# Optimization experiments

Hardware: AMD Instinct MI355X
Metric: run time of the kernel (lower is better)

## Reference

```python
import jax, jax.numpy as jnp
import numpy as np

H = 16        # attn_num
A = 64        # head dim
W = 512       # sliding-window length (ar_attn_window_len)
THETA = 10000.0
EPS = 1e-6    # norm_eps


def _rope(x):
    # x: [b, h, s, a]
    s, a = x.shape[2], x.shape[3]
    inv_freq = (1.0 / THETA) ** (jnp.arange(0, a, 2, dtype=jnp.float32) / a)
    freqs = jnp.arange(s, dtype=jnp.float32)[:, None] * inv_freq[None, :]  # [s, a/2]
    cos, sin = jnp.cos(freqs), jnp.sin(freqs)
    x1, x2 = jnp.split(x, 2, axis=-1)
    return jnp.concatenate([x1 * cos + x2 * sin, -x1 * sin + x2 * cos], axis=-1)


def _l2_normalize(x):
    # F.normalize(x, dim=-1, eps): x / max(||x||_2, eps)
    n = jnp.sqrt(jnp.sum(x * x, axis=-1, keepdims=True))
    return x / jnp.maximum(n, EPS)


def setup_inputs() -> dict:
    key = jax.random.key(0)
    kq, kk, kv = jax.random.split(key, 3)
    b, s, d = 2, 4096, H * A
    return {
        "xq": jax.random.normal(kq, (b, s, d), dtype=jnp.float32),
        "xk": jax.random.normal(kk, (b, s, d), dtype=jnp.float32),
        "xv": jax.random.normal(kv, (b, s, d), dtype=jnp.float32),
    }


def reference(xq, xk, xv):
    b, s, d = xq.shape
    to_heads = lambda x: x.reshape(b, s, H, A).transpose(0, 2, 1, 3)  # b h s a
    q, k, v = to_heads(xq), to_heads(xk), to_heads(xv)

    # qk-norm then RoPE, exactly as Attention.forward
    q = _rope(_l2_normalize(q))
    k = _rope(_l2_normalize(k))

    # Block-banded causal sliding-window attention (honors the block sparsity):
    # query block i attends only to key blocks i-1 and i (window = block size W).
    nb = s // W
    qb = q.reshape(b, H, nb, W, A)

    def band(x):
        xb = x.reshape(b, H, nb, W, A)
        xp = jnp.pad(xb, ((0, 0), (0, 0), (1, 0), (0, 0), (0, 0)))  # zero block in front
        return jnp.concatenate([xp[:, :, :-1], xp[:, :, 1:]], axis=3)  # [b,H,nb,2W,A]

    kb, vb = band(k), band(v)

    scale = 1.0 / np.sqrt(A)
    scores = jnp.einsum("bhnqa,bhnka->bhnqk", qb, kb) * scale  # [b,H,nb,W,2W]

    # mask: causal (q >= kv), window (q - kv < W), and kv index in range (>= 0)
    r = jnp.arange(W)
    c = jnp.arange(2 * W)
    diff = r[:, None] - (c[None, :] - W)               # q_global - kv_global
    within = (diff >= 0) & (diff < W)                   # [W, 2W]
    kv_global = (jnp.arange(nb)[:, None] - 1) * W + c[None, :]  # [nb, 2W]
    mask = within[None, :, :] & (kv_global[:, None, :] >= 0)    # [nb, W, 2W]

    scores = jnp.where(mask[None, None], scores, -1e30)
    p = jax.nn.softmax(scores, axis=-1)
    out = jnp.einsum("bhnqk,bhnka->bhnqa", p, vb)       # [b,H,nb,W,A]
    out = out.reshape(b, H, s, A).transpose(0, 2, 1, 3).reshape(b, s, d)
    return out
```

## Files before the change

### kernel.cpp

```cpp
#include <hip/hip_runtime.h>

#define NB 2
#define NH 16
#define SEQ 4096
#define HD 64
#define DIM 1024
#define WIN 512

typedef float f32x16 __attribute__((ext_vector_type(16)));
typedef short bf16x8 __attribute__((ext_vector_type(8)));
typedef unsigned int u32x4 __attribute__((ext_vector_type(4)));
typedef unsigned int u32x2 __attribute__((ext_vector_type(2)));
typedef unsigned short u16;
typedef unsigned int u32;

__device__ __forceinline__ u16 f2bf(float x) {
    u32 u = __float_as_uint(x);
    u += 0x7FFFu + ((u >> 16) & 1u);
    return (u16)(u >> 16);
}

__device__ __forceinline__ u32 cvtpk(float lo, float hi) {
    u32 r;
    asm("v_cvt_pk_bf16_f32 %0, %1, %2" : "=v"(r) : "v"(lo), "v"(hi));
    return r;
}

__device__ __forceinline__ float pexp2(float x) {
    return 1.f + x * (0.69314718f + x * 0.24022651f);
}

__global__ void trig_kernel(float* __restrict__ ct, float* __restrict__ st) {
    int idx = blockIdx.x * 256 + threadIdx.x;
    int s = idx >> 5, j = idx & 31;
    float inv = powf(1.0f / 10000.0f, (float)j * (1.0f / 32.0f));
    float ang = (float)s * inv;
    ct[idx] = cosf(ang);
    st[idx] = sinf(ang);
}

__device__ __forceinline__ void norm_rope_row(const float* __restrict__ row,
                                              const float* __restrict__ cr,
                                              const float* __restrict__ sr,
                                              float scale, u16* __restrict__ dst, int a) {
    float4 u0 = *(const float4*)(row + 8 * a);
    float4 u1 = *(const float4*)(row + 8 * a + 4);
    float4 v0 = *(const float4*)(row + 32 + 8 * a);
    float4 v1 = *(const float4*)(row + 32 + 8 * a + 4);
    float x1[8] = {u0.x, u0.y, u0.z, u0.w, u1.x, u1.y, u1.z, u1.w};
    float x2[8] = {v0.x, v0.y, v0.z, v0.w, v1.x, v1.y, v1.z, v1.w};
    float ss = 0.f;
#pragma unroll
    for (int i = 0; i < 8; ++i) ss += x1[i] * x1[i] + x2[i] * x2[i];
    ss += __shfl_xor(ss, 1);
    ss += __shfl_xor(ss, 2);
    float rn = scale / fmaxf(sqrtf(ss), 1e-6f);
    u16 o1[8], o2[8];
#pragma unroll
    for (int i = 0; i < 8; ++i) {
        float c = cr[8 * a + i], sn = sr[8 * a + i];
        o1[i] = f2bf((x1[i] * c + x2[i] * sn) * rn);
        o2[i] = f2bf((x2[i] * c - x1[i] * sn) * rn);
    }
    uint4 w1, w2;
    w1.x = (u32)o1[0] | ((u32)o1[1] << 16); w1.y = (u32)o1[2] | ((u32)o1[3] << 16);
    w1.z = (u32)o1[4] | ((u32)o1[5] << 16); w1.w = (u32)o1[6] | ((u32)o1[7] << 16);
    w2.x = (u32)o2[0] | ((u32)o2[1] << 16); w2.y = (u32)o2[2] | ((u32)o2[3] << 16);
    w2.z = (u32)o2[4] | ((u32)o2[5] << 16); w2.w = (u32)o2[6] | ((u32)o2[7] << 16);
    *(uint4*)(dst + 8 * a) = w1;
    *(uint4*)(dst + 32 + 8 * a) = w2;
}

__global__ void kv_prep(const float* __restrict__ xk, const float* __restrict__ xv,
                        const float* __restrict__ ctab, const float* __restrict__ stab,
                        u16* __restrict__ Kn, u16* __restrict__ Vt) {
    __shared__ u16 tile[64][66];
    int bid = blockIdx.x;
    int t = threadIdx.x;
    if (bid < 2048) {
        int bh = bid >> 6, stile = bid & 63;
        int b = bh >> 4, h = bh & 15;
        int lr = t >> 2, a = t & 3;
        int s = stile * 64 + lr;
        size_t inoff = ((size_t)(b * SEQ + s)) * DIM + h * HD;
        size_t outoff = ((size_t)bh * SEQ + s) * HD;
        norm_rope_row(xk + inoff, ctab + (size_t)s * 32, stab + (size_t)s * 32, 1.0f,
                      Kn + outoff, a);
    } else {
        int vb = bid - 2048;
        int bh = vb >> 6, stile = vb & 63;
        int b = bh >> 4, h = bh & 15;
        int lr = t >> 2, a = t & 3;
        int s = stile * 64 + lr;
        const float* vrow = xv + ((size_t)(b * SEQ + s)) * DIM + h * HD + 16 * a;
#pragma unroll
        for (int c = 0; c < 4; ++c) {
            float4 w = *(const float4*)(vrow + 4 * c);
            tile[lr][16 * a + 4 * c + 0] = f2bf(w.x);
            tile[lr][16 * a + 4 * c + 1] = f2bf(w.y);
            tile[lr][16 * a + 4 * c + 2] = f2bf(w.z);
            tile[lr][16 * a + 4 * c + 3] = f2bf(w.w);
        }
        __syncthreads();
        int d = t >> 2;
        u32 pk[8];
#pragma unroll
        for (int i = 0; i < 8; ++i) {
            u16 lo = tile[16 * a + 2 * i][d];
            u16 hi = tile[16 * a + 2 * i + 1][d];
            pk[i] = (u32)lo | ((u32)hi << 16);
        }
        u16* dst = Vt + ((size_t)bh * HD + d) * SEQ + stile * 64 + 16 * a;
        *(uint4*)(dst) = make_uint4(pk[0], pk[1], pk[2], pk[3]);
        *(uint4*)(dst + 8) = make_uint4(pk[4], pk[5], pk[6], pk[7]);
    }
}

#define KROW 72
#define VROW 40
__global__ __launch_bounds__(256, 4) void attn_kernel(const float* __restrict__ xq,
                                                      const u16* __restrict__ Kn,
                                                      const u16* __restrict__ Vt,
                                                      const float* __restrict__ ctab,
                                                      const float* __restrict__ stab,
                                                      float* __restrict__ out) {
    __shared__ __align__(16) u16 Kl[2][32 * KROW];
    __shared__ __align__(16) u16 Vl[2][64 * VROW];
    int phys = blockIdx.x;
    int logical = (phys & 7) * 128 + (phys >> 3);
    int bh = logical >> 5, qt = logical & 31;
    int b = bh >> 4, h = bh & 15;
    int tid = threadIdx.x;
    int w = tid >> 6, l = tid & 63;
    int q = l & 31, hi = l >> 5;
    int qblk = qt * 128;
    int qw0 = qblk + w * 32;
    const u16* Kh = Kn + (size_t)bh * SEQ * HD;
    const u16* Vh = Vt + (size_t)bh * HD * SEQ;
    int dq = qw0 + q;

    int bt0 = (qblk - (WIN - 1)) >> 5; if (bt0 < 0) bt0 = 0;
    int bt1 = (qblk + 96) >> 5;

    int krow = tid >> 3, kc = (tid & 7) * 8;
    int vrw  = tid >> 2, vc = (tid & 3) * 8;
    const u16* kgl = Kh + (size_t)krow * HD + kc;
    const u16* vgl = Vh + (size_t)vrw * SEQ + vc;
    u16* kls0 = &Kl[0][krow * KROW + kc];
    u16* kls1 = &Kl[1][krow * KROW + kc];
    u16* vls0 = &Vl[0][vrw * VROW + vc];
    u16* vls1 = &Vl[1][vrw * VROW + vc];

    {
        uint4 gk = *(const uint4*)(kgl + ((size_t)bt0 << 5) * HD);
        uint4 gv = *(const uint4*)(vgl + (bt0 << 5));
        *(uint4*)kls0 = gk;
        *(uint4*)vls0 = gv;
    }

    const float* qrow = xq + ((size_t)(b * SEQ + dq)) * DIM + h * HD;
    float4 xa0 = *(const float4*)(qrow + hi * 8);
    float4 xa1 = *(const float4*)(qrow + hi * 8 + 4);
    float4 xb0 = *(const float4*)(qrow + 16 + hi * 8);
    float4 xb1 = *(const float4*)(qrow + 16 + hi * 8 + 4);
    float4 ya0 = *(const float4*)(qrow + 32 + hi * 8);
    float4 ya1 = *(const float4*)(qrow + 36 + hi * 8);
    float4 yb0 = *(const float4*)(qrow + 48 + hi * 8);
    float4 yb1 = *(const float4*)(qrow + 52 + hi * 8);
    auto d4 = [](float4 v) { return v.x * v.x + v.y * v.y + v.z * v.z + v.w * v.w; };
    float ss = d4(xa0) + d4(xa1) + d4(xb0) + d4(xb1) + d4(ya0) + d4(ya1) + d4(yb0) + d4(yb1);
    ss += __shfl_xor(ss, 32);
    float rn = (0.125f * 1.44269504f) / fmaxf(sqrtf(ss), 1e-6f);
    const float* crp = ctab + (size_t)dq * 32;
    const float* srp = stab + (size_t)dq * 32;
    float4 ca0 = *(const float4*)(crp + hi * 8);
    float4 ca1 = *(const float4*)(crp + hi * 8 + 4);
    float4 cb0 = *(const float4*)(crp + 16 + hi * 8);
    float4 cb1 = *(const float4*)(crp + 16 + hi * 8 + 4);
    float4 sa0 = *(const float4*)(srp + hi * 8);
    float4 sa1 = *(const float4*)(srp + hi * 8 + 4);
    float4 sb0 = *(const float4*)(srp + 16 + hi * 8);
    float4 sb1 = *(const float4*)(srp + 16 + hi * 8 + 4);
    auto mk1 = [&](float4 x0, float4 x1f, float4 y0, float4 y1f,
                   float4 c0, float4 c1, float4 s0, float4 s1) -> bf16x8 {
        u32x4 r;
        r[0] = cvtpk((x0.x * c0.x + y0.x * s0.x) * rn, (x0.y * c0.y + y0.y * s0.y) * rn);
        r[1] = cvtpk((x0.z * c0.z + y0.z * s0.z) * rn, (x0.w * c0.w + y0.w * s0.w) * rn);
        r[2] = cvtpk((x1f.x * c1.x + y1f.x * s1.x) * rn, (x1f.y * c1.y + y1f.y * s1.y) * rn);
        r[3] = cvtpk((x1f.z * c1.z + y1f.z * s1.z) * rn, (x1f.w * c1.w + y1f.w * s1.w) * rn);
        return __builtin_bit_cast(bf16x8, r);
    };
    auto mk2 = [&](float4 x0, float4 x1f, float4 y0, float4 y1f,
                   float4 c0, float4 c1, float4 s0, float4 s1) -> bf16x8 {
        u32x4 r;
        r[0] = cvtpk((y0.x * c0.x - x0.x * s0.x) * rn, (y0.y * c0.y - x0.y * s0.y) * rn);
        r[1] = cvtpk((y0.z * c0.z - x0.z * s0.z) * rn, (y0.w * c0.w - x0.w * s0.w) * rn);
        r[2] = cvtpk((y1f.x * c1.x - x1f.x * s1.x) * rn, (y1f.y * c1.y - x1f.y * s1.y) * rn);
        r[3] = cvtpk((y1f.z * c1.z - x1f.z * s1.z) * rn, (y1f.w * c1.w - x1f.w * s1.w) * rn);
        return __builtin_bit_cast(bf16x8, r);
    };
    bf16x8 qf0 = mk1(xa0, xa1, ya0, ya1, ca0, ca1, sa0, sa1);
    bf16x8 qf1 = mk1(xb0, xb1, yb0, yb1, cb0, cb1, sb0, sb1);
    bf16x8 qf2 = mk2(xa0, xa1, ya0, ya1, ca0, ca1, sa0, sa1);
    bf16x8 qf3 = mk2(xb0, xb1, yb0, yb1, cb0, cb1, sb0, sb1);

    f32x16 acc0, acc1;
#pragma unroll
    for (int i = 0; i < 16; ++i) { acc0[i] = 0.f; acc1[i] = 0.f; }
    float l_ = 0.f;

    int tw0 = (qw0 - (WIN - 1)) >> 5; if (tw0 < 0) tw0 = 0;
    int tw1 = qw0 >> 5;

    const u16* krd0 = &Kl[0][q * KROW + hi * 8];
    const u16* krd1 = &Kl[1][q * KROW + hi * 8];
    const u16* vrd0a = &Vl[0][q * VROW + hi * 8];
    const u16* vrd0b = &Vl[0][(32 + q) * VROW + hi * 8];
    const u16* vrd1a = &Vl[1][q * VROW + hi * 8];
    const u16* vrd1b = &Vl[1][(32 + q) * VROW + hi * 8];

    __syncthreads();

    int c = 0;
    for (int t = bt0; t <= bt1; ++t) {
        int kv0 = t << 5;
        bool more = t < bt1;
        uint4 gk, gv;
        if (more) {
            gk = *(const uint4*)(kgl + ((size_t)(kv0 + 32)) * HD);
            gv = *(const uint4*)(vgl + (kv0 + 32));
        }
        __builtin_amdgcn_sched_barrier(0);

        if (t >= tw0 && t <= tw1) {
            bool mask = (t == tw0) || (t == tw1);
            const u16* kr = c ? krd1 : krd0;
            const u16* va = c ? vrd1a : vrd0a;
            const u16* vb = c ? vrd1b : vrd0b;

            bf16x8 k0 = *(const bf16x8*)(kr);
            bf16x8 k1 = *(const bf16x8*)(kr + 16);
            bf16x8 k2 = *(const bf16x8*)(kr + 32);
            bf16x8 k3 = *(const bf16x8*)(kr + 48);

            f32x16 st;
#pragma unroll
            for (int i = 0; i < 16; ++i) st[i] = 0.f;
            __builtin_amdgcn_s_setprio(1);
            st = __builtin_amdgcn_mfma_f32_32x32x16_bf16(k0, qf0, st, 0, 0, 0);
            st = __builtin_amdgcn_mfma_f32_32x32x16_bf16(k1, qf1, st, 0, 0, 0);
            st = __builtin_amdgcn_mfma_f32_32x32x16_bf16(k2, qf2, st, 0, 0, 0);
            st = __builtin_amdgcn_mfma_f32_32x32x16_bf16(k3, qf3, st, 0, 0, 0);
            __builtin_amdgcn_s_setprio(0);

            bf16x8 va0 = *(const bf16x8*)(va);
            bf16x8 va1 = *(const bf16x8*)(va + 16);
            bf16x8 vb0 = *(const bf16x8*)(vb);
            bf16x8 vb1 = *(const bf16x8*)(vb + 16);

            int base = dq - (kv0 + 4 * hi);
            u32 wd[8];
            float l0 = 0.f, l1 = 0.f;
#pragma unroll
            for (int i = 0; i < 8; ++i) {
                int r0 = 2 * i, r1 = 2 * i + 1;
                float e0 = pexp2(st[r0]);
                float e1 = pexp2(st[r1]);
                if (mask) {
                    int k0off = (r0 & 3) + 8 * (r0 >> 2);
                    int k1off = (r1 & 3) + 8 * (r1 >> 2);
                    e0 = ((u32)(base - k0off) < (u32)WIN) ? e0 : 0.f;
                    e1 = ((u32)(base - k1off) < (u32)WIN) ? e1 : 0.f;
                }
                l0 += e0; l1 += e1;
                wd[i] = cvtpk(e0, e1);
            }
            l_ += l0 + l1;

            u32x4 b1, b2;
#if __has_builtin(__builtin_amdgcn_permlane32_swap)
            u32x2 sA = __builtin_amdgcn_permlane32_swap(wd[0], wd[2], false, false);
            u32x2 sB = __builtin_amdgcn_permlane32_swap(wd[1], wd[3], false, false);
            u32x2 sC = __builtin_amdgcn_permlane32_swap(wd[4], wd[6], false, false);
            u32x2 sD = __builtin_amdgcn_permlane32_swap(wd[5], wd[7], false, false);
            b1 = (u32x4){ sA[0], sB[0], sA[1], sB[1] };
            b2 = (u32x4){ sC[0], sD[0], sC[1], sD[1] };
#else
            u32 e0 = __shfl_xor(hi ? wd[0] : wd[2], 32);
            u32 e1 = __shfl_xor(hi ? wd[1] : wd[3], 32);
            u32 e2 = __shfl_xor(hi ? wd[4] : wd[6], 32);
            u32 e3 = __shfl_xor(hi ? wd[5] : wd[7], 32);
            b1 = (u32x4){ hi ? e0 : wd[0], hi ? e1 : wd[1], hi ? wd[2] : e0, hi ? wd[3] : e1 };
            b2 = (u32x4){ hi ? e2 : wd[4], hi ? e3 : wd[5], hi ? wd[6] : e2, hi ? wd[7] : e3 };
#endif
            bf16x8 pb1 = __builtin_bit_cast(bf16x8, b1);
            bf16x8 pb2 = __builtin_bit_cast(bf16x8, b2);

            __builtin_amdgcn_s_setprio(1);
            acc0 = __builtin_amdgcn_mfma_f32_32x32x16_bf16(va0, pb1, acc0, 0, 0, 0);
            acc0 = __builtin_amdgcn_mfma_f32_32x32x16_bf16(va1, pb2, acc0, 0, 0, 0);
            acc1 = __builtin_amdgcn_mfma_f32_32x32x16_bf16(vb0, pb1, acc1, 0, 0, 0);
            acc1 = __builtin_amdgcn_mfma_f32_32x32x16_bf16(vb1, pb2, acc1, 0, 0, 0);
            __builtin_amdgcn_s_setprio(0);
        }

        if (more) {
            *(uint4*)(c ? kls0 : kls1) = gk;
            *(uint4*)(c ? vls0 : vls1) = gv;
            __syncthreads();
        }
        c ^= 1;
    }

    l_ += __shfl_xor(l_, 32);
    float inv = 1.0f / l_;
    float* orow = out + ((size_t)(b * SEQ + dq)) * DIM + h * HD;
#pragma unroll
    for (int g = 0; g < 4; ++g) {
        float4 v0 = { acc0[4 * g + 0] * inv, acc0[4 * g + 1] * inv,
                      acc0[4 * g + 2] * inv, acc0[4 * g + 3] * inv };
        float4 v1 = { acc1[4 * g + 0] * inv, acc1[4 * g + 1] * inv,
                      acc1[4 * g + 2] * inv, acc1[4 * g + 3] * inv };
        *(float4*)(orow + 8 * g + 4 * hi) = v0;
        *(float4*)(orow + 32 + 8 * g + 4 * hi) = v1;
    }
}

extern "C" void kernel_launch(void* const* d_in, const int* in_sizes, int n_in,
                              void* d_out, int out_size, void* d_ws, size_t ws_size,
                              hipStream_t stream) {
    (void)in_sizes; (void)n_in; (void)out_size; (void)ws_size;
    const float* xq = (const float*)d_in[0];
    const float* xk = (const float*)d_in[1];
    const float* xv = (const float*)d_in[2];
    float* out = (float*)d_out;

    const size_t HEADS_ELEMS = (size_t)NB * NH * SEQ * HD;
    u16* Kn = (u16*)d_ws;
    u16* Vt = Kn + HEADS_ELEMS;
    float* ctab = (float*)(Vt + HEADS_ELEMS);
    float* stab = ctab + (size_t)SEQ * 32;

    trig_kernel<<<dim3(512), dim3(256), 0, stream>>>(ctab, stab);
    kv_prep<<<dim3(4096), dim3(256), 0, stream>>>(xk, xv, ctab, stab, Kn, Vt);
    attn_kernel<<<dim3(1024), dim3(256), 0, stream>>>(xq, Kn, Vt, ctab, stab, out);
}
```

Before: 65.63 us.

## Fold trig table generation into kv_prep and compute K RoPE factors inline

Removes the separate trig_kernel launch by adding extra blocks to kv_prep that write the cos/sin tables used by the attention kernel. The K-normalization path now computes its own cos/sin values in registers instead of reading the table, which drops the dependency between the two kernels. The attention kernel's launch bounds are raised from 4 to 5 blocks per SM, which caps registers per thread and risks spills. Inline transcendental math also adds ALU work per K element.

```diff
diff --git a/kernel.cpp b/kernel.cpp
--- a/kernel.cpp
+++ b/kernel.cpp
@@ -30,19 +30,9 @@
     return 1.f + x * (0.69314718f + x * 0.24022651f);
 }
 
-__global__ void trig_kernel(float* __restrict__ ct, float* __restrict__ st) {
-    int idx = blockIdx.x * 256 + threadIdx.x;
-    int s = idx >> 5, j = idx & 31;
-    float inv = powf(1.0f / 10000.0f, (float)j * (1.0f / 32.0f));
-    float ang = (float)s * inv;
-    ct[idx] = cosf(ang);
-    st[idx] = sinf(ang);
-}
-
-__device__ __forceinline__ void norm_rope_row(const float* __restrict__ row,
-                                              const float* __restrict__ cr,
-                                              const float* __restrict__ sr,
-                                              float scale, u16* __restrict__ dst, int a) {
+__device__ __forceinline__ void norm_rope_row2(const float* __restrict__ row,
+                                               const float (&cr)[8], const float (&sr)[8],
+                                               float scale, u16* __restrict__ dst, int a) {
     float4 u0 = *(const float4*)(row + 8 * a);
     float4 u1 = *(const float4*)(row + 8 * a + 4);
     float4 v0 = *(const float4*)(row + 32 + 8 * a);
@@ -58,7 +48,7 @@
     u16 o1[8], o2[8];
 #pragma unroll
     for (int i = 0; i < 8; ++i) {
-        float c = cr[8 * a + i], sn = sr[8 * a + i];
+        float c = cr[i], sn = sr[i];
         o1[i] = f2bf((x1[i] * c + x2[i] * sn) * rn);
         o2[i] = f2bf((x2[i] * c - x1[i] * sn) * rn);
     }
@@ -72,7 +62,7 @@
 }
 
 __global__ void kv_prep(const float* __restrict__ xk, const float* __restrict__ xv,
-                        const float* __restrict__ ctab, const float* __restrict__ stab,
+                        float* __restrict__ ctab, float* __restrict__ stab,
                         u16* __restrict__ Kn, u16* __restrict__ Vt) {
     __shared__ u16 tile[64][66];
     int bid = blockIdx.x;
@@ -82,11 +72,18 @@
         int b = bh >> 4, h = bh & 15;
         int lr = t >> 2, a = t & 3;
         int s = stile * 64 + lr;
+        float c8[8], s8[8];
+#pragma unroll
+        for (int i = 0; i < 8; ++i) {
+            float invf = exp2f((float)(8 * a + i) * -0.4152410118f);
+            float ang = (float)s * invf;
+            c8[i] = cosf(ang);
+            s8[i] = sinf(ang);
+        }
         size_t inoff = ((size_t)(b * SEQ + s)) * DIM + h * HD;
         size_t outoff = ((size_t)bh * SEQ + s) * HD;
-        norm_rope_row(xk + inoff, ctab + (size_t)s * 32, stab + (size_t)s * 32, 1.0f,
-                      Kn + outoff, a);
-    } else {
+        norm_rope_row2(xk + inoff, c8, s8, 1.0f, Kn + outoff, a);
+    } else if (bid < 4096) {
         int vb = bid - 2048;
         int bh = vb >> 6, stile = vb & 63;
         int b = bh >> 4, h = bh & 15;
@@ -113,12 +110,19 @@
         u16* dst = Vt + ((size_t)bh * HD + d) * SEQ + stile * 64 + 16 * a;
         *(uint4*)(dst) = make_uint4(pk[0], pk[1], pk[2], pk[3]);
         *(uint4*)(dst + 8) = make_uint4(pk[4], pk[5], pk[6], pk[7]);
+    } else {
+        int idx = (bid - 4096) * 256 + t;
+        int s = idx >> 5, j = idx & 31;
+        float invf = exp2f((float)j * -0.4152410118f);
+        float ang = (float)s * invf;
+        ctab[idx] = cosf(ang);
+        stab[idx] = sinf(ang);
     }
 }
 
 #define KROW 72
 #define VROW 40
-__global__ __launch_bounds__(256, 4) void attn_kernel(const float* __restrict__ xq,
+__global__ __launch_bounds__(256, 5) void attn_kernel(const float* __restrict__ xq,
                                                       const u16* __restrict__ Kn,
                                                       const u16* __restrict__ Vt,
                                                       const float* __restrict__ ctab,
@@ -341,7 +345,6 @@
     float* ctab = (float*)(Vt + HEADS_ELEMS);
     float* stab = ctab + (size_t)SEQ * 32;
 
-    trig_kernel<<<dim3(512), dim3(256), 0, stream>>>(ctab, stab);
-    kv_prep<<<dim3(4096), dim3(256), 0, stream>>>(xk, xv, ctab, stab, Kn, Vt);
+    kv_prep<<<dim3(4608), dim3(256), 0, stream>>>(xk, xv, ctab, stab, Kn, Vt);
     attn_kernel<<<dim3(1024), dim3(256), 0, stream>>>(xq, Kn, Vt, ctab, stab, out);
 }
```

After: 94.30 us. 1.44x slower.
